# Kernel tuning notes

Hardware: AMD Instinct MI355X
Metric: run time of the kernel (lower is better)

The kernel has to match this reference:

```python
import jax, jax.numpy as jnp
import numpy as np
from jax.scipy.linalg import expm

DELTA = 0.01  # time step from __init__ delta
B_SZ, U_DIM, DU_DIM, H_DIM, Y_DIM = 512, 1024, 512, 2048, 1024


def setup_inputs() -> dict:
    key = jax.random.key(0)
    ks = jax.random.split(key, 6)
    inv_sqrt = lambda fan_in: 1.0 / np.sqrt(fan_in)
    u = jax.random.normal(ks[0], (B_SZ, U_DIM), jnp.float32)
    du = jax.random.normal(ks[1], (B_SZ, DU_DIM), jnp.float32)
    # torch.nn.Linear default init: U(-1/sqrt(fan_in), 1/sqrt(fan_in))
    W = jax.random.uniform(ks[2], (H_DIM, H_DIM), jnp.float32, -inv_sqrt(H_DIM), inv_sqrt(H_DIM))
    Bw = jax.random.uniform(ks[3], (H_DIM, U_DIM + DU_DIM), jnp.float32, -inv_sqrt(U_DIM + DU_DIM), inv_sqrt(U_DIM + DU_DIM))
    Cw = jax.random.uniform(ks[4], (Y_DIM, H_DIM), jnp.float32, -inv_sqrt(H_DIM), inv_sqrt(H_DIM))
    h = jax.random.normal(ks[5], (1, H_DIM), jnp.float32)
    return {"u": u, "du": du, "W": W, "Bw": Bw, "Cw": Cw, "h": h}


def reference(u, du, W, Bw, Cw, h):
    # Antisymmetric part of W
    A = 0.5 * (W - W.T)                                    # (H,H)
    A_expm = expm(A * DELTA)                               # (H,H) matrix exponential
    rec = h @ A_expm.T                                     # (1,H) recurrent term: F.linear(h, A_expm)
    A_inv = jnp.linalg.inv(A)                              # (H,H)
    # B(cat([du, u])) : (B, H)
    b = jnp.concatenate([du, u], axis=1) @ Bw.T
    # M = A^{-1} (expm(A*delta) - I); input term = M @ b^T per sample -> b @ M^T
    M = A_inv @ (A_expm - jnp.eye(H_DIM, dtype=A.dtype))   # (H,H)
    inp = b @ M.T                                          # (B,H)
    h_new = rec + inp                                      # broadcast (1,H)+(B,H) -> (B,H)
    y = h_new @ Cw.T                                       # (B,Y)
    return y
```

## Files before the change

### kernel.cpp

```cpp
#include <hip/hip_runtime.h>
#include <hip/hip_bf16.h>


#define B_SZ 512
#define U_DIM 1024
#define DU_DIM 512
#define H_DIM 2048
#define Y_DIM 1024
#define K_CAT 1536
#define DELTA_F 0.01f

typedef __hip_bfloat16 bf16;
using bf16x8f = __attribute__((ext_vector_type(8))) short;
using f32x4   = __attribute__((ext_vector_type(4))) float;

__device__ __forceinline__ short f2bs(float x) {
  union { bf16 b; short s; } u; u.b = __float2bfloat16(x); return u.s;
}
__device__ __forceinline__ int4 pack8(const float4 v0, const float4 v1) {
  union { short s[8]; int4 i; } o;
  o.s[0] = f2bs(v0.x); o.s[1] = f2bs(v0.y); o.s[2] = f2bs(v0.z); o.s[3] = f2bs(v0.w);
  o.s[4] = f2bs(v1.x); o.s[5] = f2bs(v1.y); o.s[6] = f2bs(v1.z); o.s[7] = f2bs(v1.w);
  return o.i;
}

__device__ __forceinline__ void stage16(const void* g, void* l) {
  __builtin_amdgcn_global_load_lds(
      (const __attribute__((address_space(1))) unsigned int*)g,
      (__attribute__((address_space(3))) unsigned int*)l, 16, 0, 0);
}

#define NB   (H_DIM * K_CAT / 8)
#define NCAT (B_SZ * K_CAT / 8)
#define NC   (Y_DIM * H_DIM / 8)

__global__ __launch_bounds__(256) void k1(const float* __restrict__ W, const float* __restrict__ h,
                                          const float* __restrict__ Bw, const float* __restrict__ du,
                                          const float* __restrict__ u, float* __restrict__ wh,
                                          float* __restrict__ wtp, short* __restrict__ Bwb,
                                          short* __restrict__ catb) {
  const int b = blockIdx.x;
  if (b < 512) {
    const int lane = threadIdx.x & 63, wave = threadIdx.x >> 6;
    const int row = b * 4 + wave;
    const float* wr = W + (size_t)row * H_DIM;
    float s = 0.f;
#pragma unroll
    for (int it = 0; it < 8; it++) {
      int k = it * 256 + lane * 4;
      float4 a = *(const float4*)(wr + k);
      float4 hv = *(const float4*)(h + k);
      s += a.x * hv.x + a.y * hv.y + a.z * hv.z + a.w * hv.w;
    }
#pragma unroll
    for (int off = 32; off > 0; off >>= 1) s += __shfl_down(s, off);
    if (lane == 0) wh[row] = s;
  } else if (b < 768) {
    const int e = b - 512;
    const int colg = e & 7, rowg = e >> 3;
    const int k = colg * 256 + threadIdx.x;
    float s = 0.f;
    const float* base = W + (size_t)rowg * 64 * H_DIM + k;
#pragma unroll 8
    for (int i = 0; i < 64; i++) s += base[(size_t)i * H_DIM] * h[rowg * 64 + i];
    wtp[rowg * H_DIM + k] = s;
  } else {
    for (int g = (b - 768) * 256 + threadIdx.x; g < NB + NCAT; g += 256 * 256) {
      if (g < NB) {
        int e = g * 8;
        *(int4*)(Bwb + e) = pack8(*(const float4*)(Bw + e), *(const float4*)(Bw + e + 4));
      } else {
        int g2 = g - NB;
        int row = g2 / 192, c = g2 - row * 192;
        const float* src = (c < 64) ? du + (size_t)row * DU_DIM + c * 8
                                    : u + (size_t)row * U_DIM + (c - 64) * 8;
        *(int4*)(catb + (size_t)row * K_CAT + c * 8) =
            pack8(*(const float4*)src, *(const float4*)(src + 4));
      }
    }
  }
}

#define MFMA __builtin_amdgcn_mfma_f32_16x16x32_bf16

__global__ __launch_bounds__(256) void k2(const short* __restrict__ catb, const short* __restrict__ Bwb,
                                          const float* __restrict__ h, const float* __restrict__ wh,
                                          const float* __restrict__ wtp, short* __restrict__ bb,
                                          const float* __restrict__ Cw, short* __restrict__ Cwb) {
  __shared__ __align__(16) short lds[2 * 6144];
  __shared__ float recf[64];
  const int b = blockIdx.x;
  if (b >= 512) {
    int g0 = (b - 512) * 256 + threadIdx.x;
    int e = g0 * 8;
    *(int4*)(Cwb + e) = pack8(*(const float4*)(Cw + e), *(const float4*)(Cw + e + 4));
    e = (g0 + 131072) * 8;
    *(int4*)(Cwb + e) = pack8(*(const float4*)(Cw + e), *(const float4*)(Cw + e + 4));
    return;
  }
  const int tid = threadIdx.x;
  const int lane = tid & 63, wave = tid >> 6;
  const int wm = wave >> 1, wn = wave & 1;
  const int mt = b >> 5, nt = b & 31;
  const int row0 = mt * 32, col0 = nt * 64;
  const int rA = tid >> 3, gA = tid & 7;
  const int sA = (gA ^ (rA & 7)) * 8;
  const short* srcA  = catb + (size_t)(row0 + rA) * K_CAT + sA;
  const short* srcB1 = Bwb + (size_t)(col0 + rA) * K_CAT + sA;
  const short* srcB2 = Bwb + (size_t)(col0 + 32 + rA) * K_CAT + sA;
  const int NT = K_CAT / 64;
  const int rm = lane & 15, quad = lane >> 4;
  f32x4 acc[2] = {};
  stage16(srcA,  lds + tid * 8);
  stage16(srcB1, lds + 2048 + tid * 8);
  stage16(srcB2, lds + 4096 + tid * 8);
  __syncthreads();
  const int ra = wm * 16 + rm;
  const int rb0 = wn * 32 + rm, rb1 = wn * 32 + 16 + rm;
  const int oa = ra * 64, ob0 = rb0 * 64, ob1 = rb1 * 64;
  const int xa = (ra & 7), xb0 = (rb0 & 7), xb1 = (rb1 & 7);
  for (int kt = 0; kt < NT; kt++) {
    const int cur = kt & 1;
    if (kt + 1 < NT) {
      const int o = (kt + 1) * 64;
      short* nb = lds + (cur ^ 1) * 6144;
      stage16(srcA + o,  nb + tid * 8);
      stage16(srcB1 + o, nb + 2048 + tid * 8);
      stage16(srcB2 + o, nb + 4096 + tid * 8);
    }
    const short* Ac = lds + cur * 6144;
    const short* Bc = Ac + 2048;
#pragma unroll
    for (int ks = 0; ks < 2; ks++) {
      const int kg = ks * 4 + quad;
      bf16x8f af  = *(const bf16x8f*)&Ac[oa + ((kg ^ xa) << 3)];
      bf16x8f bf0 = *(const bf16x8f*)&Bc[ob0 + ((kg ^ xb0) << 3)];
      bf16x8f bf1 = *(const bf16x8f*)&Bc[ob1 + ((kg ^ xb1) << 3)];
      acc[0] = MFMA(af, bf0, acc[0], 0, 0, 0);
      acc[1] = MFMA(af, bf1, acc[1], 0, 0, 0);
    }
    if (kt + 1 < NT) __syncthreads();
  }
  if (tid < 64) {
    int gc = col0 + tid;
    float s = 0.f;
#pragma unroll
    for (int p = 0; p < 32; p++) s += wtp[p * H_DIM + gc];
    recf[tid] = h[gc] + 0.005f * (wh[gc] - s);
  }
  __syncthreads();
#pragma unroll
  for (int j = 0; j < 2; j++) {
    int gc = col0 + wn * 32 + 16 * j + rm;
#pragma unroll
    for (int r = 0; r < 4; r++) {
      int gr = row0 + wm * 16 + quad * 4 + r;
      bb[(size_t)gr * H_DIM + gc] = f2bs(recf[gc - col0] + DELTA_F * acc[j][r]);
    }
  }
}

__global__ __launch_bounds__(256) void k3(const short* __restrict__ A, const short* __restrict__ B,
                                          float* __restrict__ y) {
  __shared__ __align__(16) short lds[2 * 4096];
  const int tid = threadIdx.x;
  const int lane = tid & 63, wave = tid >> 6;
  const int wm = wave >> 1, wn = wave & 1;
  const int mt = blockIdx.x >> 5, nt = blockIdx.x & 31;
  const int row0 = mt * 32, col0 = nt * 32;
  const int rA = tid >> 3, gA = tid & 7;
  const int sA = (gA ^ (rA & 7)) * 8;
  const short* srcA = A + (size_t)(row0 + rA) * H_DIM + sA;
  const short* srcB = B + (size_t)(col0 + rA) * H_DIM + sA;
  const int NT = H_DIM / 64;
  const int rm = lane & 15, quad = lane >> 4;
  f32x4 acc = {};
  stage16(srcA, lds + tid * 8);
  stage16(srcB, lds + 2048 + tid * 8);
  __syncthreads();
  const int ra = wm * 16 + rm, rb = wn * 16 + rm;
  const int oa = ra * 64, ob = rb * 64;
  const int xa = (ra & 7), xb = (rb & 7);
  for (int kt = 0; kt < NT; kt++) {
    const int cur = kt & 1;
    if (kt + 1 < NT) {
      const int o = (kt + 1) * 64;
      short* nb = lds + (cur ^ 1) * 4096;
      stage16(srcA + o, nb + tid * 8);
      stage16(srcB + o, nb + 2048 + tid * 8);
    }
    const short* Ac = lds + cur * 4096;
    const short* Bc = Ac + 2048;
#pragma unroll
    for (int ks = 0; ks < 2; ks++) {
      const int kg = ks * 4 + quad;
      bf16x8f af = *(const bf16x8f*)&Ac[oa + ((kg ^ xa) << 3)];
      bf16x8f bf = *(const bf16x8f*)&Bc[ob + ((kg ^ xb) << 3)];
      acc = MFMA(af, bf, acc, 0, 0, 0);
    }
    if (kt + 1 < NT) __syncthreads();
  }
  int gc = col0 + wn * 16 + rm;
#pragma unroll
  for (int r = 0; r < 4; r++) {
    int gr = row0 + wm * 16 + quad * 4 + r;
    y[(size_t)gr * Y_DIM + gc] = acc[r];
  }
}

extern "C" void kernel_launch(void* const* d_in, const int* in_sizes, int n_in,
                              void* d_out, int out_size, void* d_ws, size_t ws_size,
                              hipStream_t stream) {
  const float* u  = (const float*)d_in[0];
  const float* du = (const float*)d_in[1];
  const float* W  = (const float*)d_in[2];
  const float* Bw = (const float*)d_in[3];
  const float* Cw = (const float*)d_in[4];
  const float* h  = (const float*)d_in[5];
  float* y = (float*)d_out;

  char* w = (char*)d_ws;
  size_t off = 0;
  short* Bwb  = (short*)(w + off); off += (size_t)H_DIM * K_CAT * sizeof(short);
  short* Cwb  = (short*)(w + off); off += (size_t)Y_DIM * H_DIM * sizeof(short);
  short* bb   = (short*)(w + off); off += (size_t)B_SZ * H_DIM * sizeof(short);
  short* catb = (short*)(w + off); off += (size_t)B_SZ * K_CAT * sizeof(short);
  float* wh   = (float*)(w + off); off += H_DIM * sizeof(float);
  float* wtp  = (float*)(w + off); off += 32 * H_DIM * sizeof(float);
  if (ws_size < off) return;

  k1<<<1024, 256, 0, stream>>>(W, h, Bw, du, u, wh, wtp, Bwb, catb);
  k2<<<1024, 256, 0, stream>>>(catb, Bwb, h, wh, wtp, bb, Cw, Cwb);
  k3<<<512, 256, 0, stream>>>(bb, Cwb, y);
}
```

Before: 123.5 us.

## Triple-buffer LDS staging in GEMM kernels with vmcnt-based waits

Both MFMA GEMM kernels (k2 and k3) move from double-buffered LDS staging to a three-stage ring. Loads are issued two K-tiles ahead, and a partial s_waitcnt vmcnt plus a single raw s_barrier per iteration replaces the trailing __syncthreads. The goal is to keep more global-to-LDS traffic in flight and hide memory latency in these small-tile, latency-bound GEMMs. It costs 50% more LDS per block and relies on stage16 being direct async loads counted by vmcnt, so the hand-set wait counts have to match the number of loads per stage.

```diff
diff --git a/kernel.cpp b/kernel.cpp
--- a/kernel.cpp
+++ b/kernel.cpp
@@ -87,7 +87,7 @@
                                           const float* __restrict__ h, const float* __restrict__ wh,
                                           const float* __restrict__ wtp, short* __restrict__ bb,
                                           const float* __restrict__ Cw, short* __restrict__ Cwb) {
-  __shared__ __align__(16) short lds[2 * 6144];
+  __shared__ __align__(16) short lds[3 * 6144];
   __shared__ float recf[64];
   const int b = blockIdx.x;
   if (b >= 512) {
@@ -111,35 +111,40 @@
   const int NT = K_CAT / 64;
   const int rm = lane & 15, quad = lane >> 4;
   f32x4 acc[2] = {};
-  stage16(srcA,  lds + tid * 8);
-  stage16(srcB1, lds + 2048 + tid * 8);
-  stage16(srcB2, lds + 4096 + tid * 8);
-  __syncthreads();
+#pragma unroll
+  for (int t = 0; t < 2; t++) {
+    short* nb = lds + t * 6144;
+    const int o = t * 64;
+    stage16(srcA + o,  nb + tid * 8);
+    stage16(srcB1 + o, nb + 2048 + tid * 8);
+    stage16(srcB2 + o, nb + 4096 + tid * 8);
+  }
   const int ra = wm * 16 + rm;
   const int rb0 = wn * 32 + rm, rb1 = wn * 32 + 16 + rm;
-  const int oa = ra * 64, ob0 = rb0 * 64, ob1 = rb1 * 64;
+  const int oa = ra * 64, ob0 = 2048 + rb0 * 64, ob1 = 2048 + rb1 * 64;
   const int xa = (ra & 7), xb0 = (rb0 & 7), xb1 = (rb1 & 7);
+#pragma unroll
   for (int kt = 0; kt < NT; kt++) {
-    const int cur = kt & 1;
-    if (kt + 1 < NT) {
-      const int o = (kt + 1) * 64;
-      short* nb = lds + (cur ^ 1) * 6144;
+    if (kt < NT - 1) asm volatile("s_waitcnt vmcnt(3)" ::: "memory");
+    else             asm volatile("s_waitcnt vmcnt(0)" ::: "memory");
+    __builtin_amdgcn_s_barrier();
+    if (kt + 2 < NT) {
+      const int o = (kt + 2) * 64;
+      short* nb = lds + ((kt + 2) % 3) * 6144;
       stage16(srcA + o,  nb + tid * 8);
       stage16(srcB1 + o, nb + 2048 + tid * 8);
       stage16(srcB2 + o, nb + 4096 + tid * 8);
     }
-    const short* Ac = lds + cur * 6144;
-    const short* Bc = Ac + 2048;
+    const short* Ac = lds + (kt % 3) * 6144;
 #pragma unroll
     for (int ks = 0; ks < 2; ks++) {
       const int kg = ks * 4 + quad;
       bf16x8f af  = *(const bf16x8f*)&Ac[oa + ((kg ^ xa) << 3)];
-      bf16x8f bf0 = *(const bf16x8f*)&Bc[ob0 + ((kg ^ xb0) << 3)];
-      bf16x8f bf1 = *(const bf16x8f*)&Bc[ob1 + ((kg ^ xb1) << 3)];
+      bf16x8f bf0 = *(const bf16x8f*)&Ac[ob0 + ((kg ^ xb0) << 3)];
+      bf16x8f bf1 = *(const bf16x8f*)&Ac[ob1 + ((kg ^ xb1) << 3)];
       acc[0] = MFMA(af, bf0, acc[0], 0, 0, 0);
       acc[1] = MFMA(af, bf1, acc[1], 0, 0, 0);
     }
-    if (kt + 1 < NT) __syncthreads();
   }
   if (tid < 64) {
     int gc = col0 + tid;
@@ -162,7 +167,7 @@
 
 __global__ __launch_bounds__(256) void k3(const short* __restrict__ A, const short* __restrict__ B,
                                           float* __restrict__ y) {
-  __shared__ __align__(16) short lds[2 * 4096];
+  __shared__ __align__(16) short lds[3 * 4096];
   const int tid = threadIdx.x;
   const int lane = tid & 63, wave = tid >> 6;
   const int wm = wave >> 1, wn = wave & 1;
@@ -175,30 +180,35 @@
   const int NT = H_DIM / 64;
   const int rm = lane & 15, quad = lane >> 4;
   f32x4 acc = {};
-  stage16(srcA, lds + tid * 8);
-  stage16(srcB, lds + 2048 + tid * 8);
-  __syncthreads();
+#pragma unroll
+  for (int t = 0; t < 2; t++) {
+    short* nb = lds + t * 4096;
+    const int o = t * 64;
+    stage16(srcA + o, nb + tid * 8);
+    stage16(srcB + o, nb + 2048 + tid * 8);
+  }
   const int ra = wm * 16 + rm, rb = wn * 16 + rm;
-  const int oa = ra * 64, ob = rb * 64;
+  const int oa = ra * 64, ob = 2048 + rb * 64;
   const int xa = (ra & 7), xb = (rb & 7);
+#pragma unroll
   for (int kt = 0; kt < NT; kt++) {
-    const int cur = kt & 1;
-    if (kt + 1 < NT) {
-      const int o = (kt + 1) * 64;
-      short* nb = lds + (cur ^ 1) * 4096;
+    if (kt < NT - 1) asm volatile("s_waitcnt vmcnt(2)" ::: "memory");
+    else             asm volatile("s_waitcnt vmcnt(0)" ::: "memory");
+    __builtin_amdgcn_s_barrier();
+    if (kt + 2 < NT) {
+      const int o = (kt + 2) * 64;
+      short* nb = lds + ((kt + 2) % 3) * 4096;
       stage16(srcA + o, nb + tid * 8);
       stage16(srcB + o, nb + 2048 + tid * 8);
     }
-    const short* Ac = lds + cur * 4096;
-    const short* Bc = Ac + 2048;
+    const short* Ac = lds + (kt % 3) * 4096;
 #pragma unroll
     for (int ks = 0; ks < 2; ks++) {
       const int kg = ks * 4 + quad;
       bf16x8f af = *(const bf16x8f*)&Ac[oa + ((kg ^ xa) << 3)];
-      bf16x8f bf = *(const bf16x8f*)&Bc[ob + ((kg ^ xb) << 3)];
+      bf16x8f bf = *(const bf16x8f*)&Ac[ob + ((kg ^ xb) << 3)];
       acc = MFMA(af, bf, acc, 0, 0, 0);
     }
-    if (kt + 1 < NT) __syncthreads();
   }
   int gc = col0 + wn * 16 + rm;
 #pragma unroll
```

Result: faster. 111.4 us (-9.8%).
